# Performance work log

Measured on AMD Instinct MI355X. Metric: run time of the kernel, lower is better.

## Reference

```python
import jax, jax.numpy as jnp
import numpy as np

ROPE_DIMS = 16
NUM_HEADS = 16
NUM_KV_HEADS = 4
HEAD_DIM = 128
ROPE_BASE = 10000.0


def _rope_cos_sin(T, dtype):
    # inv_freq over rope_dims=16 -> 8 freqs; emb = cat(freqs, freqs) -> 16 cols
    inv_freq = 1.0 / (ROPE_BASE ** (jnp.arange(0, ROPE_DIMS, 2, dtype=jnp.float32) / ROPE_DIMS))
    t = jnp.arange(T, dtype=jnp.float32)
    freqs = jnp.outer(t, inv_freq)              # [T, 8]
    emb = jnp.concatenate([freqs, freqs], -1)   # [T, 16]
    return jnp.cos(emb).astype(dtype), jnp.sin(emb).astype(dtype)


def _apply_rotary(x):
    # x: [B, H, T, head_dim]; rotate only first ROPE_DIMS dims
    T = x.shape[-2]
    cos, sin = _rope_cos_sin(T, x.dtype)        # [T, 16]
    x_rope, x_pass = x[..., :ROPE_DIMS], x[..., ROPE_DIMS:]
    half = ROPE_DIMS // 2
    x1, x2 = x_rope[..., :half], x_rope[..., half:]
    rotated = jnp.concatenate([-x2, x1], -1)
    x_rope = x_rope * cos + rotated * sin
    return jnp.concatenate([x_rope, x_pass], -1)


def setup_inputs() -> dict:
    key = jax.random.key(0)
    ks = jax.random.split(key, 5)
    B, T, C = 4, 2048, 2048
    kv_out = NUM_KV_HEADS * HEAD_DIM
    s = 0.02
    return {
        "x_normed": jax.random.normal(ks[0], (B, T, C), jnp.float32),
        "q_w": jax.random.normal(ks[1], (C, C), jnp.float32) * s,
        "k_w": jax.random.normal(ks[2], (kv_out, C), jnp.float32) * s,
        "v_w": jax.random.normal(ks[3], (kv_out, C), jnp.float32) * s,
        "out_w": jax.random.normal(ks[4], (C, C), jnp.float32) * s,
        "qk_gain": jnp.ones((1, NUM_HEADS, 1, 1), jnp.float32),
    }


def reference(x_normed, q_w, k_w, v_w, out_w, qk_gain):
    B, T, C = x_normed.shape
    H, kvH, hd = NUM_HEADS, NUM_KV_HEADS, HEAD_DIM
    q = (x_normed @ q_w.T).reshape(B, T, H, hd).transpose(0, 2, 1, 3)    # [B,H,T,hd]
    k = (x_normed @ k_w.T).reshape(B, T, kvH, hd).transpose(0, 2, 1, 3)  # [B,kvH,T,hd]
    v = (x_normed @ v_w.T).reshape(B, T, kvH, hd).transpose(0, 2, 1, 3)
    q = _apply_rotary(q)
    k = _apply_rotary(k)
    q = q * qk_gain
    reps = H // kvH
    if reps > 1:
        k = jnp.repeat(k, reps, axis=1)  # [B,H,T,hd]
        v = jnp.repeat(v, reps, axis=1)
    scale = 1.0 / jnp.sqrt(jnp.asarray(hd, q.dtype))
    scores = jnp.einsum('bhqd,bhkd->bhqk', q, k) * scale
    causal = jnp.tril(jnp.ones((T, T), bool))
    scores = jnp.where(causal, scores, jnp.asarray(-jnp.inf, scores.dtype))
    probs = jax.nn.softmax(scores, axis=-1)
    attn = jnp.einsum('bhqk,bhkd->bhqd', probs, v)
    attn = attn.transpose(0, 2, 1, 3).reshape(B, T, C)
    out = attn @ out_w.T
    return out, v[:, :kvH]
```

## Files before the change

kernel.cpp:

```cpp
#include <hip/hip_runtime.h>
#include <hip/hip_bf16.h>
#include <stdint.h>
#include <math.h>

#define T_SEQ 2048
#define CDIM  2048
#define NB    4
#define NH    16
#define NKV   4
#define HD    128

typedef __attribute__((ext_vector_type(8))) short short8;
typedef __attribute__((ext_vector_type(4))) float f32x4;

__device__ __forceinline__ void gload_lds16(const void* g, void* l) {
  __builtin_amdgcn_global_load_lds((const __attribute__((address_space(1))) void*)g,
                                   (__attribute__((address_space(3))) void*)l, 16, 0, 0);
}

__device__ __forceinline__ f32x4 mfma_bf16(short8 a, short8 b, f32x4 c) {
  return __builtin_amdgcn_mfma_f32_16x16x32_bf16(a, b, c, 0, 0, 0);
}

__device__ __forceinline__ unsigned short f2bf(float x) {
  union { float f; unsigned u; } v; v.f = x;
  unsigned r = v.u + 0x7fffu + ((v.u >> 16) & 1u);
  return (unsigned short)(r >> 16);
}

__device__ __forceinline__ unsigned pk_bf16(float a, float b) {
  unsigned r;
  asm("v_cvt_pk_bf16_f32 %0, %1, %2" : "=v"(r) : "v"(a), "v"(b));
  return r;
}

__device__ __forceinline__ float exp2_fast(float x) {
  float r;
  asm("v_exp_f32 %0, %1" : "=v"(r) : "v"(x));
  return r;
}

__global__ void cvt_all(const float* __restrict__ x,  const float* __restrict__ qw,
                        const float* __restrict__ kw, const float* __restrict__ vw,
                        const float* __restrict__ ow,
                        unsigned short* __restrict__ xb,  unsigned short* __restrict__ qwb,
                        unsigned short* __restrict__ kwb, unsigned short* __restrict__ vwb,
                        unsigned short* __restrict__ owb) {
  const int bid = blockIdx.x;
  const float* src; unsigned short* dst; int base, nb, n4;
  if (bid < 2048)      { src = x;  dst = xb;  base = 0;    nb = 2048; n4 = 4194304; }
  else if (bid < 2560) { src = qw; dst = qwb; base = 2048; nb = 512;  n4 = 1048576; }
  else if (bid < 2688) { src = kw; dst = kwb; base = 2560; nb = 128;  n4 = 262144;  }
  else if (bid < 2816) { src = vw; dst = vwb; base = 2688; nb = 128;  n4 = 262144;  }
  else                 { src = ow; dst = owb; base = 2816; nb = 512;  n4 = 1048576; }
  const int stride = nb * 256;
  for (int i = (bid - base) * 256 + threadIdx.x; i < n4; i += stride) {
    float4 v = *(const float4*)(src + (size_t)i * 4);
    ushort4 o;
    o.x = f2bf(v.x); o.y = f2bf(v.y); o.z = f2bf(v.z); o.w = f2bf(v.w);
    *(ushort4*)(dst + (size_t)i * 4) = o;
  }
}

template<int MODE>
__launch_bounds__(512, 2)
__global__ void gemm256(const unsigned short* __restrict__ A,
                        const unsigned short* __restrict__ W,
                        int N, int K,
                        unsigned short* __restrict__ obf,
                        float* __restrict__ of32,
                        const float* __restrict__ gain)
{
  __shared__ alignas(16) short As[2][2][256 * 32];
  __shared__ alignas(16) short Bs[2][2][256 * 32];
  const int tid = threadIdx.x;
  const int lane = tid & 63, w = tid >> 6;
  const int wr = w >> 2, wc = w & 3;
  const int lr = lane & 15, lg = lane >> 4;

  const int nwg  = gridDim.x * gridDim.y;
  const int orig = blockIdx.y * gridDim.x + blockIdx.x;
  const int cpx  = nwg >> 3;
  const int swz  = (orig & 7) * cpx + (orig >> 3);
  const int m0 = (swz / gridDim.x) * 256, n0 = (swz % gridDim.x) * 256;

  f32x4 acc[8][4] = {};
  const int nkt = K >> 6;
  const int rsw = (lr >> 1) & 3;

  auto stageA = [&](int kt, int buf, int kk) {
#pragma unroll
    for (int i = 0; i < 2; ++i) {
      int t = i * 512 + tid;
      int row = t >> 2;
      int cs = (t & 3) ^ ((t >> 3) & 3);
      gload_lds16(A + (size_t)(m0 + row) * K + kt * 64 + kk * 32 + cs * 8,
                  (char*)&As[buf][kk][0] + i * 8192 + w * 1024);
    }
  };
  auto stageB = [&](int kt, int buf, int kk) {
#pragma unroll
    for (int i = 0; i < 2; ++i) {
      int t = i * 512 + tid;
      int row = t >> 2;
      int cs = (t & 3) ^ ((t >> 3) & 3);
      gload_lds16(W + (size_t)(n0 + row) * K + kt * 64 + kk * 32 + cs * 8,
                  (char*)&Bs[buf][kk][0] + i * 8192 + w * 1024);
    }
  };

  stageA(0, 0, 0); stageB(0, 0, 0); stageA(0, 0, 1); stageB(0, 0, 1);
  asm volatile("s_waitcnt vmcnt(4)" ::: "memory");
  __builtin_amdgcn_s_barrier();

  int cur = 0;
  for (int kt = 0; kt < nkt; ++kt) {
    const int tn = (kt + 1 < nkt) ? kt + 1 : kt;
#pragma unroll
    for (int kk = 0; kk < 2; ++kk) {
      short8 bfr[4], af[4];
#pragma unroll
      for (int fn = 0; fn < 4; ++fn) {
        int rb = wc * 64 + fn * 16 + lr;
        bfr[fn] = *(const short8*)((const char*)&Bs[cur][kk][0] + rb * 64 + ((lg ^ rsw) << 4));
      }
#pragma unroll
      for (int fm = 0; fm < 4; ++fm) {
        int ra = wr * 128 + fm * 16 + lr;
        af[fm] = *(const short8*)((const char*)&As[cur][kk][0] + ra * 64 + ((lg ^ rsw) << 4));
      }
      stageA(tn, cur ^ 1, kk);
      __builtin_amdgcn_s_barrier();
      __builtin_amdgcn_s_setprio(1);
#pragma unroll
      for (int fm = 0; fm < 4; ++fm)
#pragma unroll
        for (int fn = 0; fn < 4; ++fn)
          acc[fm][fn] = mfma_bf16(af[fm], bfr[fn], acc[fm][fn]);
      __builtin_amdgcn_s_setprio(0);
      __builtin_amdgcn_s_barrier();

#pragma unroll
      for (int fm = 0; fm < 4; ++fm) {
        int ra = wr * 128 + (4 + fm) * 16 + lr;
        af[fm] = *(const short8*)((const char*)&As[cur][kk][0] + ra * 64 + ((lg ^ rsw) << 4));
      }
      stageB(tn, cur ^ 1, kk);
      asm volatile("s_waitcnt vmcnt(4)" ::: "memory");
      __builtin_amdgcn_s_barrier();
      __builtin_amdgcn_s_setprio(1);
#pragma unroll
      for (int fm = 0; fm < 4; ++fm)
#pragma unroll
        for (int fn = 0; fn < 4; ++fn)
          acc[4 + fm][fn] = mfma_bf16(af[fm], bfr[fn], acc[4 + fm][fn]);
      __builtin_amdgcn_s_setprio(0);
      __builtin_amdgcn_s_barrier();
    }
    cur ^= 1;
  }
  asm volatile("s_waitcnt vmcnt(0)" ::: "memory");

#pragma unroll
  for (int fm = 0; fm < 8; ++fm) {
    const int mbase = m0 + wr * 128 + fm * 16 + lg * 4;
#pragma unroll
    for (int fn = 0; fn < 4; ++fn) {
      const int ncol = n0 + wc * 64 + fn * 16 + lr;
      if constexpr (MODE == 0) {
#pragma unroll
        for (int r = 0; r < 4; ++r)
          of32[(size_t)(mbase + r) * N + ncol] = acc[fm][fn][r];
      } else {
        const int hh = ncol >> 7;
        const int d  = ncol & 127;
        const bool rope = ((wc & 1) == 0) && (fn == 0);
#pragma unroll
        for (int r = 0; r < 4; ++r) {
          float val = acc[fm][fn][r];
          const int m  = mbase + r;
          const int t  = m & (T_SEQ - 1);
          const int bb = m >> 11;
          if (rope) {
            float partner = __shfl_xor(val, 8);
            float invf = exp2f(-(float)(d & 7) * 1.6609640474436813f);
            float ang = (float)t * invf;
            float sn, cn;
            sincosf(ang, &sn, &cn);
            float rot = (d < 8) ? -partner : partner;
            val = val * cn + rot * sn;
          }
          val *= gain[hh] * 0.12751742676f;
          obf[(size_t)((bb * NH + hh) * T_SEQ + t) * HD + d] = f2bf(val);
        }
      }
    }
  }
}

__launch_bounds__(256, 2)
__global__ void gemm_kv(const unsigned short* __restrict__ A,
                        const unsigned short* __restrict__ W,
                        unsigned short* __restrict__ Kout,
                        unsigned short* __restrict__ Vt,
                        float* __restrict__ vout)
{
  __shared__ alignas(16) short As[128 * 64];
  __shared__ alignas(16) short Bs[128 * 64];
  __shared__ alignas(16) short Ts[128 * 132];
  const int K = CDIM;
  const int tid = threadIdx.x;
  const int lane = tid & 63, w = tid >> 6;
  const int wr = w >> 1, wc = w & 1;
  const int lr = lane & 15, lg = lane >> 4;

  const int nwg  = gridDim.x * gridDim.y;
  const int orig = blockIdx.y * gridDim.x + blockIdx.x;
  const int cpx  = nwg >> 3;
  const int swz  = (orig & 7) * cpx + (orig >> 3);
  const int m0 = (swz / gridDim.x) * 128, n0 = (swz % gridDim.x) * 128;

  f32x4 acc[4][4] = {};

  const int nkt = K >> 6;
  for (int kt = 0; kt < nkt; ++kt) {
    __syncthreads();
#pragma unroll
    for (int q = 0; q < 4; ++q) {
      int s = (w * 4 + q) * 64 + lane;
      int row = s >> 3;
      int cs2 = (s & 7) ^ (row & 7);
      gload_lds16(A + (size_t)(m0 + row) * K + (kt << 6) + cs2 * 8,
                  (char*)As + (w * 4 + q) * 1024);
      gload_lds16(W + (size_t)(n0 + row) * K + (kt << 6) + cs2 * 8,
                  (char*)Bs + (w * 4 + q) * 1024);
    }
    __syncthreads();
#pragma unroll
    for (int ks = 0; ks < 2; ++ks) {
      short8 af[4], bfr[4];
#pragma unroll
      for (int i = 0; i < 4; ++i) {
        int ra = wr * 64 + i * 16 + lr;
        int rb = wc * 64 + i * 16 + lr;
        af[i]  = *(const short8*)(As + ra * 64 + (((ks * 4 + lg) ^ (ra & 7)) << 3));
        bfr[i] = *(const short8*)(Bs + rb * 64 + (((ks * 4 + lg) ^ (rb & 7)) << 3));
      }
#pragma unroll
      for (int i = 0; i < 4; ++i)
#pragma unroll
        for (int j = 0; j < 4; ++j)
          acc[i][j] = mfma_bf16(af[i], bfr[j], acc[i][j]);
    }
  }

  const int hh = n0 >> 7;
  const int bb = m0 >> 11;
  const int tb = m0 & (T_SEQ - 1);

  if (hh < 4) {
#pragma unroll
    for (int i = 0; i < 4; ++i) {
      const int tl = wr * 64 + i * 16 + lg * 4;
#pragma unroll
      for (int j = 0; j < 4; ++j) {
        const int d = wc * 64 + j * 16 + lr;
        const bool rope = (wc == 0) && (j == 0);
#pragma unroll
        for (int r = 0; r < 4; ++r) {
          float val = acc[i][j][r];
          const int t = tb + tl + r;
          if (rope) {
            float partner = __shfl_xor(val, 8);
            float invf = exp2f(-(float)(d & 7) * 1.6609640474436813f);
            float ang = (float)t * invf;
            float sn, cn;
            sincosf(ang, &sn, &cn);
            float rot = (d < 8) ? -partner : partner;
            val = val * cn + rot * sn;
          }
          Kout[(size_t)((bb * NKV + hh) * T_SEQ + t) * HD + d] = f2bf(val);
        }
      }
    }
  } else {
    const int hv = hh - 4;
#pragma unroll
    for (int i = 0; i < 4; ++i) {
      const int tl = wr * 64 + i * 16 + lg * 4;
#pragma unroll
      for (int j = 0; j < 4; ++j) {
        const int d = wc * 64 + j * 16 + lr;
        if (hv == 0) {
#pragma unroll
          for (int r = 0; r < 4; ++r) {
            float val = acc[i][j][r];
#pragma unroll
            for (int rep = 0; rep < NKV; ++rep)
              vout[(size_t)((bb * NKV + rep) * T_SEQ + tb + tl + r) * HD + d] = val;
          }
        }
        uint2 w2;
        w2.x = pk_bf16(acc[i][j][0], acc[i][j][1]);
        w2.y = pk_bf16(acc[i][j][2], acc[i][j][3]);
        *(uint2*)(Ts + d * 132 + tl) = w2;
      }
    }
    __syncthreads();
    const int d = tid >> 1, off = (tid & 1) * 64;
    unsigned short* dst = Vt + ((size_t)(bb * NKV + hv) * HD + d) * T_SEQ + tb + off;
    const short* srcp = Ts + d * 132 + off;
#pragma unroll
    for (int jj = 0; jj < 8; ++jj)
      *(short8*)(dst + jj * 8) = *(const short8*)(srcp + jj * 8);
  }
}

__launch_bounds__(512, 4)
__global__ void attn_fwd(const unsigned short* __restrict__ Q,
                         const unsigned short* __restrict__ Kg,
                         const unsigned short* __restrict__ Vt,
                         unsigned short* __restrict__ O)
{
  __shared__ alignas(16) short Ks[2][64 * 128];
  __shared__ alignas(16) short Vs[2][128 * 64];
  __shared__ alignas(16) short Ps[128 * 64];

  const int pairi = blockIdx.x;
  const int h = blockIdx.y, b = blockIdx.z;
  const int kvh = h >> 2;
  const int tid = threadIdx.x, lane = tid & 63, w = tid >> 6;
  const int lr = lane & 15, lg = lane >> 4;

  const unsigned short* Qb  = Q  + ((size_t)(b * NH  + h)   * T_SEQ) * HD;
  const unsigned short* Kb  = Kg + ((size_t)(b * NKV + kvh) * T_SEQ) * HD;
  const unsigned short* Vtb = Vt + ((size_t)(b * NKV + kvh) * HD) * T_SEQ;

  auto stageK = [&](int kt, int buf) {
#pragma unroll
    for (int i = 0; i < 2; ++i) {
      int s = tid + i * 512;
      int row = s >> 4, c = s & 15, cs = c ^ (row & 7);
      gload_lds16(Kb + (size_t)(kt * 64 + row) * HD + cs * 8,
                  (char*)&Ks[buf][0] + w * 1024 + i * 8192);
    }
  };
  auto stageV = [&](int kt, int buf) {
#pragma unroll
    for (int i = 0; i < 2; ++i) {
      int s = tid + i * 512;
      int row = s >> 3, c = s & 7, cs = c ^ (row & 7);
      gload_lds16(Vtb + (size_t)row * T_SEQ + kt * 64 + cs * 8,
                  (char*)&Vs[buf][0] + w * 1024 + i * 8192);
    }
  };

  auto run_seg = [&](int qtile) {
    const int q0 = qtile * 128;
    const int rw = q0 + w * 16;
    const int qg = rw + lr;
    const int dtile = rw >> 6;

    short8 qf[4];
#pragma unroll
    for (int ks = 0; ks < 4; ++ks)
      qf[ks] = *(const short8*)(Qb + (size_t)qg * HD + ks * 32 + lg * 8);

    f32x4 acc_o[8] = {};
    float lrow = 0.0f;

    const int nkt = (qtile + 1) * 2;

    stageK(0, 0);
    stageV(0, 0);
    asm volatile("s_waitcnt vmcnt(2)" ::: "memory");
    __builtin_amdgcn_s_barrier();
    int cur = 0;

    const f32x4 minit = {-16.f, -16.f, -16.f, -16.f};

    for (int kt = 0; kt < nkt; ++kt) {
      const int tn = (kt + 1 < nkt) ? kt + 1 : kt;
      stageK(tn, cur ^ 1);

      const bool active = (kt <= dtile);
      if (active) {
        const short* KL = &Ks[cur][0];
        f32x4 acc2[4] = {minit, minit, minit, minit};
        __builtin_amdgcn_s_setprio(1);
#pragma unroll
        for (int kb = 0; kb < 4; ++kb) {
          int key = kb * 16 + lr;
#pragma unroll
          for (int ks = 0; ks < 4; ++ks) {
            short8 kf = *(const short8*)(KL + key * 128 + (((ks * 4 + lg) ^ (key & 7)) << 3));
            acc2[kb] = mfma_bf16(kf, qf[ks], acc2[kb]);
          }
        }
        __builtin_amdgcn_s_setprio(0);

        const bool needmask = (kt == dtile);
        if (needmask) {
#pragma unroll
          for (int kb = 0; kb < 4; ++kb)
#pragma unroll
            for (int r = 0; r < 4; ++r)
              if (kt * 64 + kb * 16 + lg * 4 + r > qg) acc2[kb][r] = -3.0e38f;
        }

        float s0 = 0.f;
#pragma unroll
        for (int kb = 0; kb < 4; ++kb) {
          float p0 = exp2_fast(acc2[kb][0]);
          float p1 = exp2_fast(acc2[kb][1]);
          float p2 = exp2_fast(acc2[kb][2]);
          float p3 = exp2_fast(acc2[kb][3]);
          s0 += (p0 + p1) + (p2 + p3);
          uint2 w2;
          w2.x = pk_bf16(p0, p1);
          w2.y = pk_bf16(p2, p3);
          int cc = (kb * 2 + (lg >> 1)) ^ (lr & 7);
          *(uint2*)(Ps + (w * 16 + lr) * 64 + (cc << 3) + ((lg & 1) << 2)) = w2;
        }
        lrow += s0;
      }

      stageV(tn, cur ^ 1);
      asm volatile("s_waitcnt vmcnt(4)" ::: "memory");
      __builtin_amdgcn_s_barrier();

      if (active) {
        const short* VL = &Vs[cur][0];
        const int qq = w * 16 + lr;
        short8 pf0 = *(const short8*)(Ps + qq * 64 + (((0 + lg) ^ (lr & 7)) << 3));
        short8 pf1 = *(const short8*)(Ps + qq * 64 + (((4 + lg) ^ (lr & 7)) << 3));
        __builtin_amdgcn_s_setprio(1);
#pragma unroll
        for (int db = 0; db < 8; ++db) {
          int vrow = db * 16 + lr;
          short8 v0 = *(const short8*)(VL + vrow * 64 + (((0 + lg) ^ (vrow & 7)) << 3));
          short8 v1 = *(const short8*)(VL + vrow * 64 + (((4 + lg) ^ (vrow & 7)) << 3));
          acc_o[db] = mfma_bf16(v0, pf0, acc_o[db]);
          acc_o[db] = mfma_bf16(v1, pf1, acc_o[db]);
        }
        __builtin_amdgcn_s_setprio(0);
      }

      asm volatile("s_waitcnt vmcnt(2)" ::: "memory");
      __builtin_amdgcn_s_barrier();
      cur ^= 1;
    }

    asm volatile("s_waitcnt vmcnt(0)" ::: "memory");
    __builtin_amdgcn_s_barrier();

    lrow += __shfl_xor(lrow, 16);
    lrow += __shfl_xor(lrow, 32);
    float invl = 1.0f / lrow;
#pragma unroll
    for (int db = 0; db < 8; ++db) {
      uint2 o2;
      o2.x = pk_bf16(acc_o[db][0] * invl, acc_o[db][1] * invl);
      o2.y = pk_bf16(acc_o[db][2] * invl, acc_o[db][3] * invl);
      *(uint2*)(O + (size_t)(b * T_SEQ + qg) * CDIM + h * HD + db * 16 + lg * 4) = o2;
    }
  };

  run_seg(15 - pairi);
  run_seg(pairi);
}

extern "C" void kernel_launch(void* const* d_in, const int* in_sizes, int n_in,
                              void* d_out, int out_size, void* d_ws, size_t ws_size,
                              hipStream_t stream) {
  (void)in_sizes; (void)n_in; (void)out_size; (void)ws_size;
  const float* x    = (const float*)d_in[0];
  const float* qw   = (const float*)d_in[1];
  const float* kw   = (const float*)d_in[2];
  const float* vw   = (const float*)d_in[3];
  const float* ow   = (const float*)d_in[4];
  const float* gain = (const float*)d_in[5];
  float* out  = (float*)d_out;
  float* vout = out + (size_t)NB * T_SEQ * CDIM;

  char* ws = (char*)d_ws;
  unsigned short* xb  = (unsigned short*)(ws);
  unsigned short* Qb  = (unsigned short*)(ws + 33554432);
  unsigned short* Kb  = (unsigned short*)(ws + 67108864);
  unsigned short* qwb = (unsigned short*)(ws + 83886080);
  unsigned short* kwb = (unsigned short*)(ws + 92274688);
  unsigned short* vwb = (unsigned short*)(ws + 94371840);
  unsigned short* owb = (unsigned short*)(ws + 96468992);
  unsigned short* Ab  = xb;
  unsigned short* Vtb = qwb;

  cvt_all<<<3328, 256, 0, stream>>>(x, qw, kw, vw, ow, xb, qwb, kwb, vwb, owb);

  gemm256<1><<<dim3(8, 32), 512, 0, stream>>>(xb, qwb, CDIM, CDIM, Qb, nullptr, gain);
  gemm_kv<<<dim3(8, 64), 256, 0, stream>>>(xb, kwb, Kb, Vtb, vout);

  attn_fwd<<<dim3(8, 16, 4), 512, 0, stream>>>(Qb, Kb, Vtb, Ab);

  gemm256<0><<<dim3(8, 32), 512, 0, stream>>>(Ab, owb, CDIM, CDIM, nullptr, out, nullptr);
}
```

Before: 297.7 us.

## Process two query heads per attention block to share K/V tiles

Each attention workgroup now handles two query heads that share one KV head, so every K and V tile staged into LDS feeds twice as many MFMAs. The grid halves, the P buffer doubles, and launch bounds drop to 2 waves-per-EU occupancy to make room for doubled accumulators and Q fragments. Barriers also get a sched_barrier so the compiler cannot move code across them. The trade is higher register and LDS pressure, lower occupancy, and only 256 workgroups, which may underfill the GPU.

```diff
diff --git a/kernel.cpp b/kernel.cpp
--- a/kernel.cpp
+++ b/kernel.cpp
@@ -38,6 +38,11 @@
   float r;
   asm("v_exp_f32 %0, %1" : "=v"(r) : "v"(x));
   return r;
+}
+
+__device__ __forceinline__ void barrier_hard() {
+  __builtin_amdgcn_s_barrier();
+  __builtin_amdgcn_sched_barrier(0);
 }
 
 __global__ void cvt_all(const float* __restrict__ x,  const float* __restrict__ qw,
@@ -316,7 +321,7 @@
   }
 }
 
-__launch_bounds__(512, 4)
+__launch_bounds__(512, 2)
 __global__ void attn_fwd(const unsigned short* __restrict__ Q,
                          const unsigned short* __restrict__ Kg,
                          const unsigned short* __restrict__ Vt,
@@ -324,15 +329,17 @@
 {
   __shared__ alignas(16) short Ks[2][64 * 128];
   __shared__ alignas(16) short Vs[2][128 * 64];
-  __shared__ alignas(16) short Ps[128 * 64];
+  __shared__ alignas(16) short Ps[256 * 64];
 
   const int pairi = blockIdx.x;
-  const int h = blockIdx.y, b = blockIdx.z;
-  const int kvh = h >> 2;
+  const int hp = blockIdx.y, b = blockIdx.z;
+  const int kvh = hp >> 1;
+  const int h0 = kvh * 4 + (hp & 1) * 2, h1 = h0 + 1;
   const int tid = threadIdx.x, lane = tid & 63, w = tid >> 6;
   const int lr = lane & 15, lg = lane >> 4;
 
-  const unsigned short* Qb  = Q  + ((size_t)(b * NH  + h)   * T_SEQ) * HD;
+  const unsigned short* Qb0 = Q  + ((size_t)(b * NH  + h0)  * T_SEQ) * HD;
+  const unsigned short* Qb1 = Q  + ((size_t)(b * NH  + h1)  * T_SEQ) * HD;
   const unsigned short* Kb  = Kg + ((size_t)(b * NKV + kvh) * T_SEQ) * HD;
   const unsigned short* Vtb = Vt + ((size_t)(b * NKV + kvh) * HD) * T_SEQ;
 
@@ -361,20 +368,22 @@
     const int qg = rw + lr;
     const int dtile = rw >> 6;
 
-    short8 qf[4];
-#pragma unroll
-    for (int ks = 0; ks < 4; ++ks)
-      qf[ks] = *(const short8*)(Qb + (size_t)qg * HD + ks * 32 + lg * 8);
-
-    f32x4 acc_o[8] = {};
-    float lrow = 0.0f;
+    short8 qf0[4], qf1[4];
+#pragma unroll
+    for (int ks = 0; ks < 4; ++ks) {
+      qf0[ks] = *(const short8*)(Qb0 + (size_t)qg * HD + ks * 32 + lg * 8);
+      qf1[ks] = *(const short8*)(Qb1 + (size_t)qg * HD + ks * 32 + lg * 8);
+    }
+
+    f32x4 acc0[8] = {}, acc1[8] = {};
+    float lrow0 = 0.0f, lrow1 = 0.0f;
 
     const int nkt = (qtile + 1) * 2;
 
     stageK(0, 0);
     stageV(0, 0);
     asm volatile("s_waitcnt vmcnt(2)" ::: "memory");
-    __builtin_amdgcn_s_barrier();
+    barrier_hard();
     int cur = 0;
 
     const f32x4 minit = {-16.f, -16.f, -16.f, -16.f};
@@ -386,7 +395,8 @@
       const bool active = (kt <= dtile);
       if (active) {
         const short* KL = &Ks[cur][0];
-        f32x4 acc2[4] = {minit, minit, minit, minit};
+        f32x4 s0[4] = {minit, minit, minit, minit};
+        f32x4 s1[4] = {minit, minit, minit, minit};
         __builtin_amdgcn_s_setprio(1);
 #pragma unroll
         for (int kb = 0; kb < 4; ++kb) {
@@ -394,75 +404,100 @@
 #pragma unroll
           for (int ks = 0; ks < 4; ++ks) {
             short8 kf = *(const short8*)(KL + key * 128 + (((ks * 4 + lg) ^ (key & 7)) << 3));
-            acc2[kb] = mfma_bf16(kf, qf[ks], acc2[kb]);
+            s0[kb] = mfma_bf16(kf, qf0[ks], s0[kb]);
+            s1[kb] = mfma_bf16(kf, qf1[ks], s1[kb]);
           }
         }
         __builtin_amdgcn_s_setprio(0);
 
-        const bool needmask = (kt == dtile);
-        if (needmask) {
+        if (kt == dtile) {
 #pragma unroll
           for (int kb = 0; kb < 4; ++kb)
 #pragma unroll
             for (int r = 0; r < 4; ++r)
-              if (kt * 64 + kb * 16 + lg * 4 + r > qg) acc2[kb][r] = -3.0e38f;
-        }
-
-        float s0 = 0.f;
+              if (kt * 64 + kb * 16 + lg * 4 + r > qg) {
+                s0[kb][r] = -3.0e38f;
+                s1[kb][r] = -3.0e38f;
+              }
+        }
+
+        float sum0 = 0.f, sum1 = 0.f;
 #pragma unroll
         for (int kb = 0; kb < 4; ++kb) {
-          float p0 = exp2_fast(acc2[kb][0]);
-          float p1 = exp2_fast(acc2[kb][1]);
-          float p2 = exp2_fast(acc2[kb][2]);
-          float p3 = exp2_fast(acc2[kb][3]);
-          s0 += (p0 + p1) + (p2 + p3);
-          uint2 w2;
-          w2.x = pk_bf16(p0, p1);
-          w2.y = pk_bf16(p2, p3);
           int cc = (kb * 2 + (lg >> 1)) ^ (lr & 7);
-          *(uint2*)(Ps + (w * 16 + lr) * 64 + (cc << 3) + ((lg & 1) << 2)) = w2;
-        }
-        lrow += s0;
+          {
+            float p0 = exp2_fast(s0[kb][0]);
+            float p1 = exp2_fast(s0[kb][1]);
+            float p2 = exp2_fast(s0[kb][2]);
+            float p3 = exp2_fast(s0[kb][3]);
+            sum0 += (p0 + p1) + (p2 + p3);
+            uint2 w2;
+            w2.x = pk_bf16(p0, p1);
+            w2.y = pk_bf16(p2, p3);
+            *(uint2*)(Ps + (w * 16 + lr) * 64 + (cc << 3) + ((lg & 1) << 2)) = w2;
+          }
+          {
+            float p0 = exp2_fast(s1[kb][0]);
+            float p1 = exp2_fast(s1[kb][1]);
+            float p2 = exp2_fast(s1[kb][2]);
+            float p3 = exp2_fast(s1[kb][3]);
+            sum1 += (p0 + p1) + (p2 + p3);
+            uint2 w2;
+            w2.x = pk_bf16(p0, p1);
+            w2.y = pk_bf16(p2, p3);
+            *(uint2*)(Ps + (128 + w * 16 + lr) * 64 + (cc << 3) + ((lg & 1) << 2)) = w2;
+          }
+        }
+        lrow0 += sum0;
+        lrow1 += sum1;
       }
 
       stageV(tn, cur ^ 1);
       asm volatile("s_waitcnt vmcnt(4)" ::: "memory");
-      __builtin_amdgcn_s_barrier();
+      barrier_hard();
 
       if (active) {
         const short* VL = &Vs[cur][0];
-        const int qq = w * 16 + lr;
-        short8 pf0 = *(const short8*)(Ps + qq * 64 + (((0 + lg) ^ (lr & 7)) << 3));
-        short8 pf1 = *(const short8*)(Ps + qq * 64 + (((4 + lg) ^ (lr & 7)) << 3));
+        const int r0 = w * 16 + lr, r1 = 128 + w * 16 + lr;
+        short8 pf00 = *(const short8*)(Ps + r0 * 64 + (((0 + lg) ^ (lr & 7)) << 3));
+        short8 pf01 = *(const short8*)(Ps + r0 * 64 + (((4 + lg) ^ (lr & 7)) << 3));
+        short8 pf10 = *(const short8*)(Ps + r1 * 64 + (((0 + lg) ^ (lr & 7)) << 3));
+        short8 pf11 = *(const short8*)(Ps + r1 * 64 + (((4 + lg) ^ (lr & 7)) << 3));
         __builtin_amdgcn_s_setprio(1);
 #pragma unroll
         for (int db = 0; db < 8; ++db) {
           int vrow = db * 16 + lr;
           short8 v0 = *(const short8*)(VL + vrow * 64 + (((0 + lg) ^ (vrow & 7)) << 3));
           short8 v1 = *(const short8*)(VL + vrow * 64 + (((4 + lg) ^ (vrow & 7)) << 3));
-          acc_o[db] = mfma_bf16(v0, pf0, acc_o[db]);
-          acc_o[db] = mfma_bf16(v1, pf1, acc_o[db]);
+          acc0[db] = mfma_bf16(v0, pf00, acc0[db]);
+          acc0[db] = mfma_bf16(v1, pf01, acc0[db]);
+          acc1[db] = mfma_bf16(v0, pf10, acc1[db]);
+          acc1[db] = mfma_bf16(v1, pf11, acc1[db]);
         }
         __builtin_amdgcn_s_setprio(0);
       }
 
       asm volatile("s_waitcnt vmcnt(2)" ::: "memory");
-      __builtin_amdgcn_s_barrier();
+      barrier_hard();
       cur ^= 1;
     }
 
     asm volatile("s_waitcnt vmcnt(0)" ::: "memory");
-    __builtin_amdgcn_s_barrier();
-
-    lrow += __shfl_xor(lrow, 16);
-    lrow += __shfl_xor(lrow, 32);
-    float invl = 1.0f / lrow;
+    barrier_hard();
+
+    lrow0 += __shfl_xor(lrow0, 16); lrow0 += __shfl_xor(lrow0, 32);
+    lrow1 += __shfl_xor(lrow1, 16); lrow1 += __shfl_xor(lrow1, 32);
+    float inv0 = 1.0f / lrow0, inv1 = 1.0f / lrow1;
 #pragma unroll
     for (int db = 0; db < 8; ++db) {
       uint2 o2;
-      o2.x = pk_bf16(acc_o[db][0] * invl, acc_o[db][1] * invl);
-      o2.y = pk_bf16(acc_o[db][2] * invl, acc_o[db][3] * invl);
-      *(uint2*)(O + (size_t)(b * T_SEQ + qg) * CDIM + h * HD + db * 16 + lg * 4) = o2;
+      o2.x = pk_bf16(acc0[db][0] * inv0, acc0[db][1] * inv0);
+      o2.y = pk_bf16(acc0[db][2] * inv0, acc0[db][3] * inv0);
+      *(uint2*)(O + (size_t)(b * T_SEQ + qg) * CDIM + h0 * HD + db * 16 + lg * 4) = o2;
+      uint2 o3;
+      o3.x = pk_bf16(acc1[db][0] * inv1, acc1[db][1] * inv1);
+      o3.y = pk_bf16(acc1[db][2] * inv1, acc1[db][3] * inv1);
+      *(uint2*)(O + (size_t)(b * T_SEQ + qg) * CDIM + h1 * HD + db * 16 + lg * 4) = o3;
     }
   };
 
@@ -499,7 +534,7 @@
   gemm256<1><<<dim3(8, 32), 512, 0, stream>>>(xb, qwb, CDIM, CDIM, Qb, nullptr, gain);
   gemm_kv<<<dim3(8, 64), 256, 0, stream>>>(xb, kwb, Kb, Vtb, vout);
 
-  attn_fwd<<<dim3(8, 16, 4), 512, 0, stream>>>(Qb, Kb, Vtb, Ab);
+  attn_fwd<<<dim3(8, 8, 4), 512, 0, stream>>>(Qb, Kb, Vtb, Ab);
 
   gemm256<0><<<dim3(8, 32), 512, 0, stream>>>(Ab, owb, CDIM, CDIM, nullptr, out, nullptr);
 }
```

After: 294.1 us. No clear change (-1.2%).
